# Kernel tuning notes

Hardware: AMD Instinct MI355X
Metric: run time of the kernel (lower is better)

## Reference

```python
import jax, jax.numpy as jnp
import numpy as np

B, E, D_IN, D = 4096, 8, 768, 768  # batch, num_domains, bert hidden, d_model


def setup_inputs() -> dict:
    key = jax.random.key(0)
    ks = jax.random.split(key, 10)
    rn = lambda k, sh: jax.random.normal(k, sh, dtype=jnp.float32) * 0.02
    zeros = lambda sh: jnp.zeros(sh, dtype=jnp.float32)
    return {
        "pooled": jax.random.normal(ks[0], (B, D_IN), dtype=jnp.float32),
        "domain_ids": jax.random.randint(ks[1], (B,), 0, E),
        # text_feature_extractor: Linear(768, d_model) + ReLU
        "W_tfe": rn(ks[2], (D_IN, D)), "b_tfe": zeros((D,)),
        # DomainFeatureExtractor per domain: FFN_1, FFN_2 (d->d each)
        "W1": rn(ks[3], (E, D, D)), "b1": zeros((E, D)),
        "W2": rn(ks[4], (E, D, D)), "b2": zeros((E, D)),
        # AdaptiveGate per domain: linear_1, linear_2 (d->d), gate_linear (2d->1)
        "G1": rn(ks[5], (E, D, D)), "g1b": zeros((E, D)),
        "G2": rn(ks[6], (E, D, D)), "g2b": zeros((E, D)),
        "Gg": rn(ks[7], (E, 2 * D)), "ggb": zeros((E,)),
    }


def reference(pooled, domain_ids, W_tfe, b_tfe, W1, b1, W2, b2,
              G1, g1b, G2, g2b, Gg, ggb):
    # text feature extractor (dropout = identity in eval)
    x = jax.nn.relu(pooled @ W_tfe + b_tfe)                        # [B, D]

    # Dense dispatch: compute every expert for every sample, then select.
    # Same math as the per-sample python loop in the torch module.
    h = jax.nn.relu(jnp.einsum('bd,edh->beh', x, W1) + b1)         # [B, E, D]
    df = jnp.einsum('beh,ehk->bek', h, W2) + b2                    # [B, E, D]

    # AdaptiveGate
    t = jax.nn.relu(jnp.einsum('bd,edh->beh', x, G1) + g1b)        # [B, E, D]
    dr = jax.nn.relu(jnp.einsum('bed,edh->beh', df, G2) + g2b)     # [B, E, D]
    # gate_linear on concat([t, dr]) == t @ Gg[:, :D] + dr @ Gg[:, D:]
    gl = (jnp.einsum('bed,ed->be', t, Gg[:, :D])
          + jnp.einsum('bed,ed->be', dr, Gg[:, D:]) + ggb)         # [B, E]
    gate = jax.nn.sigmoid(gl)                                      # [B, E]

    # route: pick this sample's domain expert
    b_idx = jnp.arange(x.shape[0])
    df_s = df[b_idx, domain_ids]                                   # [B, D]
    g_s = gate[b_idx, domain_ids][:, None]                         # [B, 1]

    final_feature = g_s * df_s + (1.0 - g_s) * x                   # [B, D]
    return final_feature
```

## Files before the change

### kernel.cpp

```cpp
#include <hip/hip_runtime.h>
#include <stdint.h>

#define BATCH 4096
#define NEXP 8
#define DIM 768
#define BM 64
#define BN 128
#define BK 32
#define MAXROWS (BATCH + NEXP * BM)
#define ROWBLKS (MAXROWS / BM)
#define MATELEMS (DIM * DIM)

typedef __attribute__((ext_vector_type(4))) float f32x4;
typedef __attribute__((ext_vector_type(8))) __bf16 bf16x8;
typedef __attribute__((ext_vector_type(8))) unsigned short ushort8v;
typedef __attribute__((ext_vector_type(4))) unsigned short ushort4v;

__device__ __forceinline__ unsigned short f2bf(float f) {
  union { float f; unsigned u; } v; v.f = f;
  unsigned r = v.u + 0x7FFFu + ((v.u >> 16) & 1u);
  return (unsigned short)(r >> 16);
}
__device__ __forceinline__ float bf2f(unsigned short h) {
  union { unsigned u; float f; } v; v.u = ((unsigned)h) << 16;
  return v.f;
}

__global__ __launch_bounds__(256) void k_transpose(
    const float* __restrict__ Wtfe, const float* __restrict__ W1,
    const float* __restrict__ W2, const float* __restrict__ G1,
    const float* __restrict__ G2, unsigned short* __restrict__ dst)
{
  __shared__ unsigned short lds[64][72];
  const int m = blockIdx.y;
  const float* src;
  if (m == 0)      src = Wtfe;
  else if (m < 9)  src = W1 + (size_t)(m - 1) * MATELEMS;
  else if (m < 17) src = W2 + (size_t)(m - 9) * MATELEMS;
  else if (m < 25) src = G1 + (size_t)(m - 17) * MATELEMS;
  else             src = G2 + (size_t)(m - 25) * MATELEMS;
  unsigned short* d = dst + (size_t)m * MATELEMS;
  const int r0 = (blockIdx.x / 12) * 64;
  const int c0 = (blockIdx.x % 12) * 64;
  const int t = threadIdx.x;
#pragma unroll
  for (int p = 0; p < 4; ++p) {
    int ri = p * 16 + (t >> 4);
    int ci = (t & 15) * 4;
    float4 v = *(const float4*)(src + (size_t)(r0 + ri) * DIM + c0 + ci);
    lds[ri][ci + 0] = f2bf(v.x);
    lds[ri][ci + 1] = f2bf(v.y);
    lds[ri][ci + 2] = f2bf(v.z);
    lds[ri][ci + 3] = f2bf(v.w);
  }
  __syncthreads();
#pragma unroll
  for (int p = 0; p < 2; ++p) {
    int jj = p * 32 + (t >> 3);
    int ii0 = (t & 7) * 8;
    ushort8v o;
#pragma unroll
    for (int u = 0; u < 8; ++u) o[u] = lds[ii0 + u][jj];
    *(ushort8v*)(d + (size_t)(c0 + jj) * DIM + r0 + ii0) = o;
  }
}

__global__ __launch_bounds__(256) void k_sort(const int* __restrict__ dom,
                                              int* __restrict__ seg,
                                              int* __restrict__ perm,
                                              float* __restrict__ gl) {
  __shared__ int cnt[8], cur[8], pstart[9];
  const int t = threadIdx.x;
  if (t < 8) { cnt[t] = 0; cur[t] = 0; }
  __syncthreads();
  for (int b = t; b < BATCH; b += 256) atomicAdd(&cnt[dom[b]], 1);
  __syncthreads();
  if (t == 0) {
    int acc = 0;
    for (int e = 0; e < 8; ++e) {
      pstart[e] = acc;
      acc += (cnt[e] + BM - 1) / BM * BM;
    }
    pstart[8] = acc;
    for (int e = 0; e < 9; ++e) seg[e] = pstart[e];
    for (int e = 0; e < 8; ++e) seg[9 + e] = cnt[e];
  }
  __syncthreads();
  for (int i = t; i < MAXROWS; i += 256) { perm[i] = 0; gl[i] = 0.0f; }
  __syncthreads();
  for (int b = t; b < BATCH; b += 256) {
    int e = dom[b];
    int pos = pstart[e] + atomicAdd(&cur[e], 1);
    perm[pos] = b;
  }
}

template <int MODE>
__global__ __launch_bounds__(256) void k_gemm(
    const void* __restrict__ Ain,
    const unsigned short* __restrict__ Wa,
    const float* __restrict__ ba,
    const unsigned short* __restrict__ Wb,
    const float* __restrict__ bb,
    const float* __restrict__ Gg,
    const int* __restrict__ seg,
    const int* __restrict__ perm,
    unsigned short* __restrict__ Out,
    float* __restrict__ gl)
{
  __shared__ __align__(16) unsigned short lA[BM * BK];
  __shared__ __align__(16) unsigned short lB[BN * BK];

  const int i0 = blockIdx.x * BM;
  if (i0 >= seg[8]) return;
  int e = 0;
#pragma unroll
  for (int q = 1; q < 8; ++q) if (i0 >= seg[q]) e = q;

  const bool isgate = (MODE == 3) || (MODE == 1 && blockIdx.y >= 6);
  const int n0 = (MODE == 1 ? (int)(blockIdx.y % 6) : (int)blockIdx.y) * BN;

  const unsigned short* We;
  const float* bias;
  if (MODE == 0) { We = Wa; bias = ba; }
  else if (MODE == 1) {
    We = (isgate ? Wb : Wa) + (size_t)e * MATELEMS;
    bias = (isgate ? bb : ba) + e * DIM;
  } else {
    We = Wa + (size_t)e * MATELEMS;
    bias = ba + e * DIM;
  }

  const int t = threadIdx.x;
  const int lane = t & 63;
  const int w = t >> 6;
  const int wr = w >> 1, wc = w & 1;
  const int srow = lane >> 2;
  const int colb = (lane & 3) * 8;

  const int arow_l = w * 16 + srow;
  const int garow = (MODE == 0) ? perm[i0 + arow_l] : (i0 + arow_l);

  const unsigned short* Abf = (const unsigned short*)Ain;
  const float* Af32 = (const float*)Ain;

  const int fr = lane & 15;
  const int sl = lane >> 4;
  const int kg = sl * 8;

  f32x4 acc[2][4];
#pragma unroll
  for (int mi = 0; mi < 2; ++mi)
#pragma unroll
    for (int ni = 0; ni < 4; ++ni) acc[mi][ni] = f32x4{0.f, 0.f, 0.f, 0.f};

  for (int kk = 0; kk < DIM; kk += BK) {
    ushort8v ta, tb[2];
    if (MODE == 0) {
      float4 va0 = *(const float4*)(Af32 + (size_t)garow * DIM + kk + colb);
      float4 va1 = *(const float4*)(Af32 + (size_t)garow * DIM + kk + colb + 4);
      ta = ushort8v{ f2bf(va0.x), f2bf(va0.y), f2bf(va0.z), f2bf(va0.w),
                     f2bf(va1.x), f2bf(va1.y), f2bf(va1.z), f2bf(va1.w) };
    } else {
      ta = *(const ushort8v*)(Abf + (size_t)garow * DIM + kk + colb);
    }
#pragma unroll
    for (int c = 0; c < 2; ++c) {
      int brow = n0 + (w * 2 + c) * 16 + srow;
      tb[c] = *(const ushort8v*)(We + (size_t)brow * DIM + kk + colb);
    }
    __syncthreads();
    *(ushort8v*)(lA + arow_l * 32 + colb) = ta;
#pragma unroll
    for (int c = 0; c < 2; ++c)
      *(ushort8v*)(lB + ((w * 2 + c) * 16 + srow) * 32 + colb) = tb[c];
    __syncthreads();

    bf16x8 af[2], bfv[4];
#pragma unroll
    for (int mi = 0; mi < 2; ++mi) {
      ushort8v raw = *(const ushort8v*)(lA + (wr * 32 + mi * 16 + fr) * 32 + kg);
      af[mi] = __builtin_bit_cast(bf16x8, raw);
    }
#pragma unroll
    for (int ni = 0; ni < 4; ++ni) {
      ushort8v raw = *(const ushort8v*)(lB + (wc * 64 + ni * 16 + fr) * 32 + kg);
      bfv[ni] = __builtin_bit_cast(bf16x8, raw);
    }
#pragma unroll
    for (int mi = 0; mi < 2; ++mi)
#pragma unroll
      for (int ni = 0; ni < 4; ++ni)
        acc[mi][ni] = __builtin_amdgcn_mfma_f32_16x16x32_bf16(af[mi], bfv[ni], acc[mi][ni], 0, 0, 0);
  }

  const int rg = sl * 4;
  if (!isgate) {
#pragma unroll
    for (int mi = 0; mi < 2; ++mi) {
#pragma unroll
      for (int ni = 0; ni < 4; ++ni) {
        int gcol = n0 + wc * 64 + ni * 16 + fr;
        float bv = bias[gcol];
#pragma unroll
        for (int r = 0; r < 4; ++r) {
          int go = i0 + wr * 32 + mi * 16 + rg + r;
          float v = acc[mi][ni][r] + bv;
          if (MODE != 2) v = fmaxf(v, 0.0f);
          Out[(size_t)go * DIM + gcol] = f2bf(v);
        }
      }
    }
  } else {
    const int goff = (MODE == 3) ? DIM : 0;
    float psum[2][4];
#pragma unroll
    for (int mi = 0; mi < 2; ++mi)
#pragma unroll
      for (int r = 0; r < 4; ++r) psum[mi][r] = 0.0f;
#pragma unroll
    for (int mi = 0; mi < 2; ++mi) {
#pragma unroll
      for (int ni = 0; ni < 4; ++ni) {
        int gcol = n0 + wc * 64 + ni * 16 + fr;
        float bv = bias[gcol];
        float gg = Gg[e * 2 * DIM + goff + gcol];
#pragma unroll
        for (int r = 0; r < 4; ++r)
          psum[mi][r] += fmaxf(acc[mi][ni][r] + bv, 0.0f) * gg;
      }
    }
#pragma unroll
    for (int s = 1; s < 16; s <<= 1)
#pragma unroll
      for (int mi = 0; mi < 2; ++mi)
#pragma unroll
        for (int r = 0; r < 4; ++r)
          psum[mi][r] += __shfl_xor(psum[mi][r], s, 64);
    if (fr == 0) {
#pragma unroll
      for (int mi = 0; mi < 2; ++mi)
#pragma unroll
        for (int r = 0; r < 4; ++r)
          atomicAdd(&gl[i0 + wr * 32 + mi * 16 + rg + r], psum[mi][r]);
    }
  }
}

__global__ __launch_bounds__(256) void k_blend(
    const int* __restrict__ seg, const int* __restrict__ perm,
    const float* __restrict__ gl, const float* __restrict__ ggb,
    const unsigned short* __restrict__ xbf, const unsigned short* __restrict__ dfbf,
    float* __restrict__ out)
{
  int idx = blockIdx.x * 256 + threadIdx.x;
  int i = idx / 192;
  int q = idx % 192;
  if (i >= seg[8]) return;
  int e = 0;
#pragma unroll
  for (int p = 1; p < 8; ++p) if (i >= seg[p]) e = p;
  if (i - seg[e] >= seg[9 + e]) return;
  int b = perm[i];
  float z = gl[i] + ggb[e];
  float g = 1.0f / (1.0f + __expf(-z));
  ushort4v dv = *(const ushort4v*)(dfbf + (size_t)i * DIM + q * 4);
  ushort4v xv = *(const ushort4v*)(xbf + (size_t)i * DIM + q * 4);
  float4 o;
  o.x = g * bf2f(dv[0]) + (1.0f - g) * bf2f(xv[0]);
  o.y = g * bf2f(dv[1]) + (1.0f - g) * bf2f(xv[1]);
  o.z = g * bf2f(dv[2]) + (1.0f - g) * bf2f(xv[2]);
  o.w = g * bf2f(dv[3]) + (1.0f - g) * bf2f(xv[3]);
  *(float4*)(out + (size_t)b * DIM + q * 4) = o;
}

extern "C" void kernel_launch(void* const* d_in, const int* in_sizes, int n_in,
                              void* d_out, int out_size, void* d_ws, size_t ws_size,
                              hipStream_t stream)
{
  const float* pooled = (const float*)d_in[0];
  const int*   dom    = (const int*)d_in[1];
  const float* Wtfe   = (const float*)d_in[2];
  const float* btfe   = (const float*)d_in[3];
  const float* W1     = (const float*)d_in[4];
  const float* b1     = (const float*)d_in[5];
  const float* W2     = (const float*)d_in[6];
  const float* b2     = (const float*)d_in[7];
  const float* G1     = (const float*)d_in[8];
  const float* g1b    = (const float*)d_in[9];
  const float* G2     = (const float*)d_in[10];
  const float* g2b    = (const float*)d_in[11];
  const float* Gg     = (const float*)d_in[12];
  const float* ggb    = (const float*)d_in[13];
  float* out = (float*)d_out;

  char* w = (char*)d_ws;
  size_t o = 0;
  auto alloc = [&](size_t bytes) { char* p = w + o; o += (bytes + 255) & ~(size_t)255; return p; };
  int*            seg  = (int*)alloc(64 * 4);
  int*            perm = (int*)alloc(MAXROWS * 4);
  float*          gl   = (float*)alloc(MAXROWS * 4);
  unsigned short* wt   = (unsigned short*)alloc((size_t)33 * MATELEMS * 2);
  unsigned short* xbf  = (unsigned short*)alloc((size_t)MAXROWS * DIM * 2);
  unsigned short* hbf  = (unsigned short*)alloc((size_t)MAXROWS * DIM * 2);
  unsigned short* dfbf = (unsigned short*)alloc((size_t)MAXROWS * DIM * 2);
  if (o > ws_size) return;

  k_transpose<<<dim3(144, 33), 256, 0, stream>>>(Wtfe, W1, W2, G1, G2, wt);
  k_sort<<<1, 256, 0, stream>>>(dom, seg, perm, gl);

  const unsigned short* wt0  = wt;
  const unsigned short* wt1  = wt + (size_t)1  * MATELEMS;
  const unsigned short* wt2  = wt + (size_t)9  * MATELEMS;
  const unsigned short* wtg1 = wt + (size_t)17 * MATELEMS;
  const unsigned short* wtg2 = wt + (size_t)25 * MATELEMS;

  k_gemm<0><<<dim3(ROWBLKS, 6),  256, 0, stream>>>(pooled, wt0,  btfe, nullptr, nullptr, Gg, seg, perm, xbf,  gl);
  k_gemm<1><<<dim3(ROWBLKS, 12), 256, 0, stream>>>(xbf,    wt1,  b1,   wtg1,    g1b,     Gg, seg, perm, hbf,  gl);
  k_gemm<2><<<dim3(ROWBLKS, 6),  256, 0, stream>>>(hbf,    wt2,  b2,   nullptr, nullptr, Gg, seg, perm, dfbf, gl);
  k_gemm<3><<<dim3(ROWBLKS, 6),  256, 0, stream>>>(dfbf,   wtg2, g2b,  nullptr, nullptr, Gg, seg, perm, nullptr, gl);

  k_blend<<<(MAXROWS * 192 + 255) / 256, 256, 0, stream>>>(seg, perm, gl, ggb, xbf, dfbf, out);
}
```

Before: 260.7 us.

## Prefetch next K tile into registers, remap blocks across XCDs, merge sort kernel

The GEMM main loop now issues the global loads for the next K tile right after the LDS stores, so memory latency overlaps the MFMA work on the current tile (register double-buffering). Block IDs are remapped so consecutive blocks are spread over the 8 XCD chunks, aiming for better L2 locality of expert weights. The separate sort kernel is folded into the transpose kernel as an extra grid row, which saves one launch. The cost is extra registers held across iterations, and the remap assumes the grid size divides evenly by 8.

New measurement: 236.9 us. 9.1% less time.

```diff
diff --git a/kernel.cpp b/kernel.cpp
--- a/kernel.cpp
+++ b/kernel.cpp
@@ -7,6 +7,7 @@
 #define BM 64
 #define BN 128
 #define BK 32
+#define NT (DIM / BK)
 #define MAXROWS (BATCH + NEXP * BM)
 #define ROWBLKS (MAXROWS / BM)
 #define MATELEMS (DIM * DIM)
@@ -26,13 +27,45 @@
   return v.f;
 }
 
-__global__ __launch_bounds__(256) void k_transpose(
+__global__ __launch_bounds__(256) void k_transpose_sort(
     const float* __restrict__ Wtfe, const float* __restrict__ W1,
     const float* __restrict__ W2, const float* __restrict__ G1,
-    const float* __restrict__ G2, unsigned short* __restrict__ dst)
+    const float* __restrict__ G2, unsigned short* __restrict__ dst,
+    const int* __restrict__ dom, int* __restrict__ seg,
+    int* __restrict__ perm, float* __restrict__ gl)
 {
   __shared__ unsigned short lds[64][72];
+  __shared__ int cnt[8], cur[8], pstart[9];
+  const int t = threadIdx.x;
   const int m = blockIdx.y;
+
+  if (m == 33) {
+    if (blockIdx.x != 0) return;
+    if (t < 8) { cnt[t] = 0; cur[t] = 0; }
+    __syncthreads();
+    for (int b = t; b < BATCH; b += 256) atomicAdd(&cnt[dom[b]], 1);
+    __syncthreads();
+    if (t == 0) {
+      int acc = 0;
+      for (int e = 0; e < 8; ++e) {
+        pstart[e] = acc;
+        acc += (cnt[e] + BM - 1) / BM * BM;
+      }
+      pstart[8] = acc;
+      for (int e = 0; e < 9; ++e) seg[e] = pstart[e];
+      for (int e = 0; e < 8; ++e) seg[9 + e] = cnt[e];
+    }
+    __syncthreads();
+    for (int i = t; i < MAXROWS; i += 256) { perm[i] = 0; gl[i] = 0.0f; }
+    __syncthreads();
+    for (int b = t; b < BATCH; b += 256) {
+      int e = dom[b];
+      int pos = pstart[e] + atomicAdd(&cur[e], 1);
+      perm[pos] = b;
+    }
+    return;
+  }
+
   const float* src;
   if (m == 0)      src = Wtfe;
   else if (m < 9)  src = W1 + (size_t)(m - 1) * MATELEMS;
@@ -42,7 +75,6 @@
   unsigned short* d = dst + (size_t)m * MATELEMS;
   const int r0 = (blockIdx.x / 12) * 64;
   const int c0 = (blockIdx.x % 12) * 64;
-  const int t = threadIdx.x;
 #pragma unroll
   for (int p = 0; p < 4; ++p) {
     int ri = p * 16 + (t >> 4);
@@ -62,36 +94,6 @@
 #pragma unroll
     for (int u = 0; u < 8; ++u) o[u] = lds[ii0 + u][jj];
     *(ushort8v*)(d + (size_t)(c0 + jj) * DIM + r0 + ii0) = o;
-  }
-}
-
-__global__ __launch_bounds__(256) void k_sort(const int* __restrict__ dom,
-                                              int* __restrict__ seg,
-                                              int* __restrict__ perm,
-                                              float* __restrict__ gl) {
-  __shared__ int cnt[8], cur[8], pstart[9];
-  const int t = threadIdx.x;
-  if (t < 8) { cnt[t] = 0; cur[t] = 0; }
-  __syncthreads();
-  for (int b = t; b < BATCH; b += 256) atomicAdd(&cnt[dom[b]], 1);
-  __syncthreads();
-  if (t == 0) {
-    int acc = 0;
-    for (int e = 0; e < 8; ++e) {
-      pstart[e] = acc;
-      acc += (cnt[e] + BM - 1) / BM * BM;
-    }
-    pstart[8] = acc;
-    for (int e = 0; e < 9; ++e) seg[e] = pstart[e];
-    for (int e = 0; e < 8; ++e) seg[9 + e] = cnt[e];
-  }
-  __syncthreads();
-  for (int i = t; i < MAXROWS; i += 256) { perm[i] = 0; gl[i] = 0.0f; }
-  __syncthreads();
-  for (int b = t; b < BATCH; b += 256) {
-    int e = dom[b];
-    int pos = pstart[e] + atomicAdd(&cur[e], 1);
-    perm[pos] = b;
   }
 }
 
@@ -111,14 +113,21 @@
   __shared__ __align__(16) unsigned short lA[BM * BK];
   __shared__ __align__(16) unsigned short lB[BN * BK];
 
-  const int i0 = blockIdx.x * BM;
+  const int nx = gridDim.x;
+  const int fid = (int)blockIdx.y * nx + (int)blockIdx.x;
+  const int chunk = (nx * (int)gridDim.y) >> 3;
+  const int nid = (fid & 7) * chunk + (fid >> 3);
+  const int bx = nid % nx;
+  const int by = nid / nx;
+
+  const int i0 = bx * BM;
   if (i0 >= seg[8]) return;
   int e = 0;
 #pragma unroll
   for (int q = 1; q < 8; ++q) if (i0 >= seg[q]) e = q;
 
-  const bool isgate = (MODE == 3) || (MODE == 1 && blockIdx.y >= 6);
-  const int n0 = (MODE == 1 ? (int)(blockIdx.y % 6) : (int)blockIdx.y) * BN;
+  const bool isgate = (MODE == 3) || (MODE == 1 && by >= 6);
+  const int n0 = (MODE == 1 ? (by % 6) : by) * BN;
 
   const unsigned short* We;
   const float* bias;
@@ -140,6 +149,8 @@
 
   const int arow_l = w * 16 + srow;
   const int garow = (MODE == 0) ? perm[i0 + arow_l] : (i0 + arow_l);
+  const int browl0 = (w * 2 + 0) * 16 + srow;
+  const int browl1 = (w * 2 + 1) * 16 + srow;
 
   const unsigned short* Abf = (const unsigned short*)Ain;
   const float* Af32 = (const float*)Ain;
@@ -154,27 +165,40 @@
 #pragma unroll
     for (int ni = 0; ni < 4; ++ni) acc[mi][ni] = f32x4{0.f, 0.f, 0.f, 0.f};
 
-  for (int kk = 0; kk < DIM; kk += BK) {
-    ushort8v ta, tb[2];
+  ushort8v ta, tb0, tb1;
+  {
     if (MODE == 0) {
-      float4 va0 = *(const float4*)(Af32 + (size_t)garow * DIM + kk + colb);
-      float4 va1 = *(const float4*)(Af32 + (size_t)garow * DIM + kk + colb + 4);
+      float4 va0 = *(const float4*)(Af32 + (size_t)garow * DIM + colb);
+      float4 va1 = *(const float4*)(Af32 + (size_t)garow * DIM + colb + 4);
       ta = ushort8v{ f2bf(va0.x), f2bf(va0.y), f2bf(va0.z), f2bf(va0.w),
                      f2bf(va1.x), f2bf(va1.y), f2bf(va1.z), f2bf(va1.w) };
     } else {
-      ta = *(const ushort8v*)(Abf + (size_t)garow * DIM + kk + colb);
-    }
-#pragma unroll
-    for (int c = 0; c < 2; ++c) {
-      int brow = n0 + (w * 2 + c) * 16 + srow;
-      tb[c] = *(const ushort8v*)(We + (size_t)brow * DIM + kk + colb);
-    }
+      ta = *(const ushort8v*)(Abf + (size_t)garow * DIM + colb);
+    }
+    tb0 = *(const ushort8v*)(We + (size_t)(n0 + browl0) * DIM + colb);
+    tb1 = *(const ushort8v*)(We + (size_t)(n0 + browl1) * DIM + colb);
+  }
+
+  for (int tt = 0; tt < NT; ++tt) {
     __syncthreads();
     *(ushort8v*)(lA + arow_l * 32 + colb) = ta;
-#pragma unroll
-    for (int c = 0; c < 2; ++c)
-      *(ushort8v*)(lB + ((w * 2 + c) * 16 + srow) * 32 + colb) = tb[c];
-    __syncthreads();
+    *(ushort8v*)(lB + browl0 * 32 + colb) = tb0;
+    *(ushort8v*)(lB + browl1 * 32 + colb) = tb1;
+    __syncthreads();
+
+    if (tt + 1 < NT) {
+      const int kn = (tt + 1) * BK;
+      if (MODE == 0) {
+        float4 va0 = *(const float4*)(Af32 + (size_t)garow * DIM + kn + colb);
+        float4 va1 = *(const float4*)(Af32 + (size_t)garow * DIM + kn + colb + 4);
+        ta = ushort8v{ f2bf(va0.x), f2bf(va0.y), f2bf(va0.z), f2bf(va0.w),
+                       f2bf(va1.x), f2bf(va1.y), f2bf(va1.z), f2bf(va1.w) };
+      } else {
+        ta = *(const ushort8v*)(Abf + (size_t)garow * DIM + kn + colb);
+      }
+      tb0 = *(const ushort8v*)(We + (size_t)(n0 + browl0) * DIM + kn + colb);
+      tb1 = *(const ushort8v*)(We + (size_t)(n0 + browl1) * DIM + kn + colb);
+    }
 
     bf16x8 af[2], bfv[4];
 #pragma unroll
@@ -306,8 +330,8 @@
   unsigned short* dfbf = (unsigned short*)alloc((size_t)MAXROWS * DIM * 2);
   if (o > ws_size) return;
 
-  k_transpose<<<dim3(144, 33), 256, 0, stream>>>(Wtfe, W1, W2, G1, G2, wt);
-  k_sort<<<1, 256, 0, stream>>>(dom, seg, perm, gl);
+  k_transpose_sort<<<dim3(144, 34), 256, 0, stream>>>(Wtfe, W1, W2, G1, G2, wt,
+                                                      dom, seg, perm, gl);
 
   const unsigned short* wt0  = wt;
   const unsigned short* wt1  = wt + (size_t)1  * MATELEMS;
```
